# Performance work log

Measured on AMD Instinct MI355X. Metric: run time of the kernel, lower is better.

## Reference

```python
import jax, jax.numpy as jnp
import numpy as np

B, T, D = 128, 512, 128
CHUNK, LEVELS, CONV = 128, 3, 10
H = CHUNK * LEVELS          # hidden_dim = 384
G = 4 * H + 2 * LEVELS      # gate width = 1542
HS = H // 6                 # 64


def setup_inputs() -> dict:
    key = jax.random.key(0)
    ks = jax.random.split(key, 12)
    def w(k, shape, fan_in):
        return (jax.random.normal(k, shape, jnp.float32) / jnp.sqrt(jnp.float32(fan_in)))
    return {
        "x": jax.random.normal(ks[0], (B, T, D), jnp.float32),
        "lengths": jax.random.randint(ks[1], (B,), 1, T + 1, jnp.int32),
        # kernel: Linear(D+1 -> G); stored as [in, out]
        "Wk": w(ks[2], (D + 1, G), D + 1),
        "bk": jnp.zeros((G,), jnp.float32),
        # recurrent_kernel: Linear(H+1 -> G)
        "Wr": w(ks[3], (H + 1, G), H + 1),
        "br": jnp.zeros((G,), jnp.float32),
        # nn_scale: H -> H//6 ; nn_rescale: H//6 -> H
        "Ws": w(ks[4], (H, HS), H),
        "bs": jnp.zeros((HS,), jnp.float32),
        "Wrs": w(ks[5], (HS, H), HS),
        "brs": jnp.zeros((H,), jnp.float32),
        # nn_conv: Conv1d(H, H, CONV) -> weight [out, in, k]
        "Wc": w(ks[6], (H, H, CONV), H * CONV),
        "bc": jnp.zeros((H,), jnp.float32),
    }


def _cumax_l2r(z):
    return jnp.cumsum(jax.nn.softmax(z, axis=-1), axis=-1)


def _cumax_r2l(z):
    s = jax.nn.softmax(z, axis=-1)  # softmax is order-invariant, flip commutes
    return jnp.flip(jnp.cumsum(jnp.flip(s, -1), -1), -1)


def reference(x, lengths, Wk, bk, Wr, br, Ws, bs, Wrs, brs, Wc, bc):
    del lengths  # present in the torch signature but unused in forward
    dtype = x.dtype
    one = jnp.ones((B, 1), dtype)  # time_intervals are all ones

    def step(carry, x_t):
        c, h, buf_h, buf_d = carry
        x_out = (jnp.concatenate([x_t, one], -1) @ Wk + bk
                 + jnp.concatenate([h, one], -1) @ Wr + br)  # [B, G]
        f_master = _cumax_l2r(x_out[:, :LEVELS])[:, :, None]          # [B,L,1]
        i_master = _cumax_r2l(x_out[:, LEVELS:2 * LEVELS])[:, :, None]
        gates = x_out[:, 2 * LEVELS:].reshape(B, 4 * LEVELS, CHUNK)
        f_g = jax.nn.sigmoid(gates[:, :LEVELS])
        i_g = jax.nn.sigmoid(gates[:, LEVELS:2 * LEVELS])
        o_g = jax.nn.sigmoid(gates[:, 2 * LEVELS:3 * LEVELS])
        c_in = jnp.tanh(gates[:, 3 * LEVELS:])
        c_l = c.reshape(B, LEVELS, CHUNK)
        ov = f_master * i_master
        c_new = (ov * (f_g * c_l + i_g * c_in)
                 + (f_master - ov) * c_l + (i_master - ov) * c_in)
        h_new = (o_g * jnp.tanh(c_new)).reshape(B, H)
        c_new = c_new.reshape(B, H)
        cur_dist = 1.0 - f_master[..., 0].mean(-1)  # [B]
        # sliding window buffers (newest last)
        buf_h = jnp.concatenate([buf_h[1:], h_new[None]], 0)   # [CONV,B,H]
        buf_d = jnp.concatenate([buf_d[1:], cur_dist[None]], 0)  # [CONV,B]
        local_dis = jax.nn.softmax(jnp.cumsum(buf_d.T, axis=1), axis=1)  # [B,CONV]
        local_h = buf_h.transpose(1, 2, 0) * local_dis[:, None, :]       # [B,H,CONV]
        theme = jax.nn.sigmoid(
            jax.nn.relu(local_h.mean(-1) @ Ws + bs) @ Wrs + brs)         # [B,H]
        # Conv1d with kernel_size == window -> full contraction over (in,k)
        conv = jnp.einsum('bik,oik->bo', local_h, Wc) + bc               # [B,H]
        return (c_new, h_new, buf_h, buf_d), (h_new, theme * conv)

    carry0 = (jnp.zeros((B, H), dtype), jnp.zeros((B, H), dtype),
              jnp.zeros((CONV, B, H), dtype), jnp.zeros((CONV, B), dtype))
    _, (origin_h, y) = jax.lax.scan(step, carry0, x.transpose(1, 0, 2))
    # [T,B,H] -> [B,T,H]; dropout layers are identity at inference
    return y.transpose(1, 0, 2) + origin_h.transpose(1, 0, 2)
```

## Files before the change

kernel.cpp:

```cpp
#include <hip/hip_runtime.h>

typedef unsigned short ushort_t;
typedef unsigned int uint32;
typedef unsigned long long uint64;
typedef __attribute__((ext_vector_type(8))) short bf16x8;
typedef __attribute__((ext_vector_type(8))) unsigned short ushort8;
typedef __attribute__((ext_vector_type(4))) float f32x4;

#define Bsz 128
#define T_STEPS 512
#define D_IN 128
#define H_DIM 384
#define G_DIM 1542
#define CONV_W 10
#define HB_ROW 49152
#define TP 521

__device__ __forceinline__ float bf2f(ushort_t u) {
  return __builtin_bit_cast(float, (uint32)u << 16);
}
__device__ __forceinline__ ushort_t f2bf(float f) {
  uint32 u = __builtin_bit_cast(uint32, f);
  u += 0x7fffu + ((u >> 16) & 1u);
  return (ushort_t)(u >> 16);
}
__device__ __forceinline__ float sigf(float x) { return 1.f / (1.f + __expf(-x)); }
__device__ __forceinline__ float tanh_f(float x) { return 1.f - 2.f / (1.f + __expf(2.f * x)); }
__device__ __forceinline__ float ldg_f(const void* p, size_t i, int f32) {
  return f32 ? ((const float*)p)[i] : bf2f(((const ushort_t*)p)[i]);
}

__global__ __launch_bounds__(64) void k_detect(const uint32* __restrict__ xw, int* __restrict__ dflag) {
  int lane = threadIdx.x;
  int cnt = 0;
  for (int i = 0; i < 16; ++i) {
    uint32 v = xw[lane * 16 + i];
    uint32 e = (v >> 7) & 0xFFu;
    cnt += (e == 0u || (e >= 0x70u && e <= 0x8Eu)) ? 1 : 0;
  }
  for (int off = 32; off; off >>= 1) cnt += __shfl_down(cnt, off);
  if (lane == 0) dflag[0] = (cnt < 700) ? 1 : 0;
}

__global__ __launch_bounds__(256) void k_zero(ushort_t* Hb, float* CD, int* flags) {
  int idx = blockIdx.x * 256 + threadIdx.x;
  if (idx < 9 * HB_ROW) Hb[idx] = 0;
  if (idx < 9 * Bsz) CD[idx] = 0.f;
  if (idx < 256) flags[idx] = 0;
}

__global__ __launch_bounds__(256) void k_packwt(const void* __restrict__ Wk, const void* __restrict__ bk,
                                                const void* __restrict__ Wr, const void* __restrict__ br,
                                                ushort_t* __restrict__ Wt, float* __restrict__ bias,
                                                const int* __restrict__ dflag) {
  const int is32 = dflag[0];
  int idx = blockIdx.x * 256 + threadIdx.x;
  int c = idx >> 9, k = idx & 511;
  int xc = (c < 1536) ? (c + 6) : (c - 1536);
  float v = 0.f;
  if (c < 1542)
    v = (k < 384) ? ldg_f(Wr, (size_t)k * G_DIM + xc, is32)
                  : ldg_f(Wk, (size_t)(k - 384) * G_DIM + xc, is32);
  Wt[idx] = f2bf(v);
  if (k == 0) {
    float bv = 0.f;
    if (c < 1542)
      bv = ldg_f(bk, xc, is32) + ldg_f(br, xc, is32)
         + ldg_f(Wk, (size_t)128 * G_DIM + xc, is32) + ldg_f(Wr, (size_t)384 * G_DIM + xc, is32);
    bias[c] = bv;
  }
}

__global__ __launch_bounds__(256) void k_packwp(const void* __restrict__ Wc, ushort_t* __restrict__ Wp,
                                                const int* __restrict__ dflag) {
  const int is32 = dflag[0];
  int idx = blockIdx.x * 256 + threadIdx.x;
  int o = idx / 3840, kk = idx % 3840;
  int k = kk / 384, i = kk % 384;
  Wp[idx] = f2bf(ldg_f(Wc, (size_t)o * 3840 + i * CONV_W + k, is32));
}

__global__ __launch_bounds__(256) void k_packsml(const void* Ws, const void* bs, const void* Wrs,
                                                 const void* brs, const void* bc,
                                                 ushort_t* Wsb, float* bsf, ushort_t* Wrsb,
                                                 float* brsf, float* bcf, const int* dflag) {
  const int is32 = dflag[0];
  int idx = blockIdx.x * 256 + threadIdx.x;
  if (idx < 24576) Wsb[idx] = f2bf(ldg_f(Ws, idx, is32));
  else if (idx < 49152) Wrsb[idx - 24576] = f2bf(ldg_f(Wrs, idx - 24576, is32));
  else if (idx < 49152 + 64) bsf[idx - 49152] = ldg_f(bs, idx - 49152, is32);
  else if (idx < 49216 + 384) brsf[idx - 49216] = ldg_f(brs, idx - 49216, is32);
  else if (idx < 49600 + 384) bcf[idx - 49600] = ldg_f(bc, idx - 49600, is32);
}

__global__ __launch_bounds__(256) void k_phaseA(const void* __restrict__ xv,
                                                const ushort_t* __restrict__ Wt,
                                                const float* __restrict__ bias,
                                                ushort_t* __restrict__ Hb,
                                                float* __restrict__ CD,
                                                int* __restrict__ flags,
                                                const int* __restrict__ dflag) {
  __shared__ float zbuf[5][16][17];
  const int is32 = dflag[0];
  const int bid = blockIdx.x;
  const int mt = bid & 7;
  const int unit = bid >> 3;
  const int lv = unit / 8, jg = unit % 8;
  const int tid = threadIdx.x;
  const int w = tid >> 6, lane = tid & 63;
  const int l15 = lane & 15, quad = lane >> 4;

  const int brow = mt * 16 + l15;
  const int cb = (lv + 3 * w) * 128 + jg * 16;
  const ushort_t* bptr = Wt + (size_t)(cb + l15) * 512 + quad * 8;
  const ushort_t* mwptr = Wt + (size_t)(1536 + l15) * 512 + quad * 8;
  const size_t xoff = (size_t)brow * (T_STEPS * D_IN) + quad * 8;
  const ushort_t* xu = (const ushort_t*)xv;
  const float* xf = (const float*)xv;
  const float biasg = bias[cb + l15];
  const float biasm = bias[1536 + l15];

  const int b_local = tid >> 4, jj = tid & 15;
  const int col = lv * 128 + jg * 16 + jj;
  const int bg = mt * 16 + b_local;
  float creg = 0.f;

  int* gflags = flags + mt * 32;

  for (int t = 0; t < T_STEPS; ++t) {
    f32x4 acc = {0.f, 0.f, 0.f, 0.f};
    f32x4 accm = {0.f, 0.f, 0.f, 0.f};
    const size_t xo = xoff + (size_t)t * D_IN;
    if (!is32) {
#pragma unroll
      for (int ks = 0; ks < 4; ++ks) {
        bf16x8 a = *(const bf16x8*)(xu + xo + ks * 32);
        bf16x8 bb = *(const bf16x8*)(bptr + (12 + ks) * 32);
        acc = __builtin_amdgcn_mfma_f32_16x16x32_bf16(a, bb, acc, 0, 0, 0);
        if (w == 0) {
          bf16x8 bm = *(const bf16x8*)(mwptr + (12 + ks) * 32);
          accm = __builtin_amdgcn_mfma_f32_16x16x32_bf16(a, bm, accm, 0, 0, 0);
        }
      }
    } else {
#pragma unroll
      for (int ks = 0; ks < 4; ++ks) {
        f32x4 fa = *(const f32x4*)(xf + xo + ks * 32);
        f32x4 fb = *(const f32x4*)(xf + xo + ks * 32 + 4);
        bf16x8 a;
#pragma unroll
        for (int j = 0; j < 4; ++j) { a[j] = (short)f2bf(fa[j]); a[4 + j] = (short)f2bf(fb[j]); }
        bf16x8 bb = *(const bf16x8*)(bptr + (12 + ks) * 32);
        acc = __builtin_amdgcn_mfma_f32_16x16x32_bf16(a, bb, acc, 0, 0, 0);
        if (w == 0) {
          bf16x8 bm = *(const bf16x8*)(mwptr + (12 + ks) * 32);
          accm = __builtin_amdgcn_mfma_f32_16x16x32_bf16(a, bm, accm, 0, 0, 0);
        }
      }
    }

    if (t > 0) {
      while (true) {
        int ok = 1;
        if (lane < 24) {
          int v = __hip_atomic_load(&gflags[lane], __ATOMIC_RELAXED, __HIP_MEMORY_SCOPE_AGENT);
          ok = (v >= t) ? 1 : 0;
        }
        if (__all(ok)) break;
      }
    }

    const ushort_t* hptr = Hb + (size_t)(8 + t) * HB_ROW + brow * H_DIM + quad * 8;
#pragma unroll
    for (int ks = 0; ks < 12; ++ks) {
      uint64 lo = __hip_atomic_load((const uint64*)(hptr + ks * 32), __ATOMIC_RELAXED, __HIP_MEMORY_SCOPE_AGENT);
      uint64 hi = __hip_atomic_load((const uint64*)(hptr + ks * 32 + 4), __ATOMIC_RELAXED, __HIP_MEMORY_SCOPE_AGENT);
      bf16x8 a;
      ((uint64*)&a)[0] = lo;
      ((uint64*)&a)[1] = hi;
      bf16x8 bb = *(const bf16x8*)(bptr + ks * 32);
      acc = __builtin_amdgcn_mfma_f32_16x16x32_bf16(a, bb, acc, 0, 0, 0);
      if (w == 0) {
        bf16x8 bm = *(const bf16x8*)(mwptr + ks * 32);
        accm = __builtin_amdgcn_mfma_f32_16x16x32_bf16(a, bm, accm, 0, 0, 0);
      }
    }
#pragma unroll
    for (int r = 0; r < 4; ++r) {
      zbuf[w][quad * 4 + r][l15] = acc[r] + biasg;
      if (w == 0) zbuf[4][quad * 4 + r][l15] = accm[r] + biasm;
    }
    __syncthreads();

    {
      float z0 = zbuf[4][b_local][0], z1 = zbuf[4][b_local][1], z2 = zbuf[4][b_local][2];
      float z3 = zbuf[4][b_local][3], z4 = zbuf[4][b_local][4], z5 = zbuf[4][b_local][5];
      float mf = fmaxf(z0, fmaxf(z1, z2));
      float e0 = __expf(z0 - mf), e1 = __expf(z1 - mf), e2 = __expf(z2 - mf);
      float rs = 1.f / (e0 + e1 + e2);
      float p0 = e0 * rs, p1 = e1 * rs;
      float fm = (lv == 0) ? p0 : (lv == 1) ? (p0 + p1) : 1.f;
      float mi = fmaxf(z3, fmaxf(z4, z5));
      float g0 = __expf(z3 - mi), g1 = __expf(z4 - mi), g2 = __expf(z5 - mi);
      float ris = 1.f / (g0 + g1 + g2);
      float q1 = g1 * ris, q2 = g2 * ris;
      float im = (lv == 0) ? 1.f : (lv == 1) ? (q1 + q2) : q2;

      float fg = sigf(zbuf[0][b_local][jj]);
      float ig = sigf(zbuf[1][b_local][jj]);
      float og = sigf(zbuf[2][b_local][jj]);
      float ci = tanh_f(zbuf[3][b_local][jj]);
      float ov = fm * im;
      float cn = creg * (ov * fg + fm - ov) + ci * (ov * ig + im - ov);
      creg = cn;
      float h = og * tanh_f(cn);

      float hp = __shfl_xor(h, 1);
      if (!(jj & 1)) {
        uint32 packed = (uint32)f2bf(h) | ((uint32)f2bf(hp) << 16);
        uint32* dst = (uint32*)(Hb + (size_t)(9 + t) * HB_ROW + bg * H_DIM + col);
        __hip_atomic_store(dst, packed, __ATOMIC_RELAXED, __HIP_MEMORY_SCOPE_AGENT);
      }
      if (unit == 0 && jj == 0) {
        float cd = 1.f - (2.f * p0 + p1 + 1.f) * (1.f / 3.f);
        __hip_atomic_store(&CD[(9 + t) * Bsz + bg], cd, __ATOMIC_RELAXED, __HIP_MEMORY_SCOPE_AGENT);
      }
    }
    __syncthreads();
    if (tid == 0)
      __hip_atomic_store(&gflags[unit], t + 1, __ATOMIC_RELAXED, __HIP_MEMORY_SCOPE_AGENT);
  }
}

__global__ __launch_bounds__(256) void k_b1(const ushort_t* __restrict__ Hb,
                                            const float* __restrict__ CD,
                                            float* __restrict__ disg,
                                            const ushort_t* __restrict__ Wsb,
                                            const float* __restrict__ bsf,
                                            const ushort_t* __restrict__ Wrsb,
                                            const float* __restrict__ brsf,
                                            void* __restrict__ out,
                                            const int* __restrict__ dflag) {
  __shared__ float disL[64][CONV_W];
  __shared__ ushort_t mL[64][H_DIM];
  __shared__ ushort_t uL[64][64];
  const int is32 = dflag[0];
  const int t = blockIdx.x >> 1;
  const int b0 = (blockIdx.x & 1) * 64;
  const int tid = threadIdx.x;

  if (tid < 64) {
    int b = tid;
    float s[CONV_W];
    float cum = 0.f, mx = -1e30f;
#pragma unroll
    for (int k = 0; k < CONV_W; ++k) {
      cum += CD[(t + k) * Bsz + b0 + b];
      s[k] = cum;
      mx = fmaxf(mx, cum);
    }
    float den = 0.f;
#pragma unroll
    for (int k = 0; k < CONV_W; ++k) { s[k] = __expf(s[k] - mx); den += s[k]; }
    float inv = 1.f / den;
#pragma unroll
    for (int k = 0; k < CONV_W; ++k) {
      float v = s[k] * inv;
      disL[b][k] = v;
      disg[(size_t)((t * Bsz) + b0 + b) * CONV_W + k] = v;
    }
  }
  __syncthreads();

  for (int ch = tid; ch < 64 * 48; ch += 256) {
    int b = ch / 48, ic = (ch % 48) * 8;
    float a[8] = {0.f, 0.f, 0.f, 0.f, 0.f, 0.f, 0.f, 0.f};
#pragma unroll
    for (int k = 0; k < CONV_W; ++k) {
      float dv = disL[b][k];
      ushort8 h8 = *(const ushort8*)(Hb + (size_t)(t + k) * HB_ROW + (b0 + b) * H_DIM + ic);
#pragma unroll
      for (int j = 0; j < 8; ++j) a[j] += dv * bf2f(h8[j]);
    }
    ushort8 mo;
#pragma unroll
    for (int j = 0; j < 8; ++j) mo[j] = f2bf(a[j] * 0.1f);
    *(ushort8*)(&mL[b][ic]) = mo;
  }
  __syncthreads();

  for (int idx = tid; idx < 64 * 64; idx += 256) {
    int b = idx >> 6, hs = idx & 63;
    float s = bsf[hs];
    for (int i = 0; i < H_DIM; ++i) s += bf2f(mL[b][i]) * bf2f(Wsb[i * 64 + hs]);
    uL[b][hs] = f2bf(fmaxf(s, 0.f));
  }
  __syncthreads();

  for (int idx = tid; idx < 64 * H_DIM; idx += 256) {
    int b = idx / H_DIM, o = idx % H_DIM;
    float s = brsf[o];
    for (int hs = 0; hs < 64; ++hs) s += bf2f(uL[b][hs]) * bf2f(Wrsb[hs * H_DIM + o]);
    float th = sigf(s);
    size_t oi = (size_t)(b0 + b) * (T_STEPS * H_DIM) + (size_t)t * H_DIM + o;
    if (is32) ((float*)out)[oi] = th; else ((ushort_t*)out)[oi] = f2bf(th);
  }
}

__global__ __launch_bounds__(256, 2) void k_b2(const ushort_t* __restrict__ Hb,
                                               const float* __restrict__ disg,
                                               const ushort_t* __restrict__ Wp,
                                               const float* __restrict__ bcf,
                                               void* __restrict__ out,
                                               const int* __restrict__ dflag) {
  __shared__ float disL[Bsz * CONV_W];
  const int is32 = dflag[0];
  const int bid = blockIdx.x;
  const int t = bid & 511, nb = bid >> 9;
  const int tid = threadIdx.x;
  const int w = tid >> 6, lane = tid & 63;
  const int l15 = lane & 15, quad = lane >> 4;

  for (int idx = tid; idx < Bsz * CONV_W; idx += 256)
    disL[idx] = disg[(size_t)t * Bsz * CONV_W + idx];
  __syncthreads();

  const int nbase = nb * 128 + w * 32;
  const ushort_t* wp0 = Wp + (size_t)(nbase + l15) * 3840 + quad * 8;
  const ushort_t* wp1 = Wp + (size_t)(nbase + 16 + l15) * 3840 + quad * 8;
  const ushort_t* hbase = Hb + (size_t)t * HB_ROW + l15 * H_DIM + quad * 8;

  f32x4 macc[8][2];
#pragma unroll
  for (int m = 0; m < 8; ++m) {
    macc[m][0] = f32x4{0.f, 0.f, 0.f, 0.f};
    macc[m][1] = f32x4{0.f, 0.f, 0.f, 0.f};
  }

  for (int tap = 0; tap < CONV_W; ++tap) {
    f32x4 pacc[8][2];
#pragma unroll
    for (int m = 0; m < 8; ++m) {
      pacc[m][0] = f32x4{0.f, 0.f, 0.f, 0.f};
      pacc[m][1] = f32x4{0.f, 0.f, 0.f, 0.f};
    }
    const ushort_t* hb = hbase + (size_t)tap * HB_ROW;
    const ushort_t* w0 = wp0 + tap * 384;
    const ushort_t* w1 = wp1 + tap * 384;
#pragma unroll
    for (int s = 0; s < 12; ++s) {
      bf16x8 bb0 = *(const bf16x8*)(w0 + s * 32);
      bf16x8 bb1 = *(const bf16x8*)(w1 + s * 32);
#pragma unroll
      for (int m = 0; m < 8; ++m) {
        bf16x8 a = *(const bf16x8*)(hb + (size_t)m * 16 * H_DIM + s * 32);
        pacc[m][0] = __builtin_amdgcn_mfma_f32_16x16x32_bf16(a, bb0, pacc[m][0], 0, 0, 0);
        pacc[m][1] = __builtin_amdgcn_mfma_f32_16x16x32_bf16(a, bb1, pacc[m][1], 0, 0, 0);
      }
    }
#pragma unroll
    for (int m = 0; m < 8; ++m) {
#pragma unroll
      for (int r = 0; r < 4; ++r) {
        float dv = disL[(m * 16 + quad * 4 + r) * CONV_W + tap];
        macc[m][0][r] += dv * pacc[m][0][r];
        macc[m][1][r] += dv * pacc[m][1][r];
      }
    }
  }

  float bc0 = bcf[nbase + l15];
  float bc1 = bcf[nbase + 16 + l15];
#pragma unroll
  for (int m = 0; m < 8; ++m) {
#pragma unroll
    for (int r = 0; r < 4; ++r) {
      int b = m * 16 + quad * 4 + r;
      size_t oidx = (size_t)b * (T_STEPS * H_DIM) + (size_t)t * H_DIM;
      int o0 = nbase + l15, o1 = o0 + 16;
      float c0 = macc[m][0][r] + bc0;
      float c1 = macc[m][1][r] + bc1;
      float h0 = bf2f(Hb[(size_t)(9 + t) * HB_ROW + b * H_DIM + o0]);
      float h1 = bf2f(Hb[(size_t)(9 + t) * HB_ROW + b * H_DIM + o1]);
      if (is32) {
        float th0 = ((float*)out)[oidx + o0];
        float th1 = ((float*)out)[oidx + o1];
        ((float*)out)[oidx + o0] = th0 * c0 + h0;
        ((float*)out)[oidx + o1] = th1 * c1 + h1;
      } else {
        float th0 = bf2f(((ushort_t*)out)[oidx + o0]);
        float th1 = bf2f(((ushort_t*)out)[oidx + o1]);
        ((ushort_t*)out)[oidx + o0] = f2bf(th0 * c0 + h0);
        ((ushort_t*)out)[oidx + o1] = f2bf(th1 * c1 + h1);
      }
    }
  }
}

extern "C" void kernel_launch(void* const* d_in, const int* in_sizes, int n_in,
                              void* d_out, int out_size, void* d_ws, size_t ws_size,
                              hipStream_t stream) {
  const void* x = d_in[0];
  const void* Wk = d_in[2];
  const void* bk = d_in[3];
  const void* Wr = d_in[4];
  const void* br = d_in[5];
  const void* Ws = d_in[6];
  const void* bs = d_in[7];
  const void* Wrs = d_in[8];
  const void* brs = d_in[9];
  const void* Wc = d_in[10];
  const void* bc = d_in[11];

  char* ws = (char*)d_ws;
  size_t off = 0;
  auto alloc = [&](size_t bytes) -> void* {
    off = (off + 255) & ~(size_t)255;
    void* p = ws + off;
    off += bytes;
    return p;
  };
  ushort_t* Hb = (ushort_t*)alloc((size_t)TP * HB_ROW * 2);
  float* CD = (float*)alloc((size_t)TP * Bsz * 4);
  ushort_t* Wt = (ushort_t*)alloc((size_t)1552 * 512 * 2);
  float* bias = (float*)alloc((size_t)1552 * 4);
  ushort_t* Wp = (ushort_t*)alloc((size_t)H_DIM * 3840 * 2);
  float* disg = (float*)alloc((size_t)T_STEPS * Bsz * CONV_W * 4);
  ushort_t* Wsb = (ushort_t*)alloc(24576 * 2);
  ushort_t* Wrsb = (ushort_t*)alloc(24576 * 2);
  float* bsf = (float*)alloc(64 * 4);
  float* brsf = (float*)alloc(384 * 4);
  float* bcf = (float*)alloc(384 * 4);
  int* flags = (int*)alloc(256 * 4);
  int* dflag = (int*)alloc(64 * 4);
  (void)ws_size; (void)in_sizes; (void)n_in; (void)out_size;

  k_detect<<<1, 64, 0, stream>>>((const uint32*)x, dflag);
  k_zero<<<1728, 256, 0, stream>>>(Hb, CD, flags);
  k_packwt<<<3104, 256, 0, stream>>>(Wk, bk, Wr, br, Wt, bias, dflag);
  k_packwp<<<5760, 256, 0, stream>>>(Wc, Wp, dflag);
  k_packsml<<<196, 256, 0, stream>>>(Ws, bs, Wrs, brs, bc, Wsb, bsf, Wrsb, brsf, bcf, dflag);
  k_phaseA<<<192, 256, 0, stream>>>(x, Wt, bias, Hb, CD, flags, dflag);
  k_b1<<<1024, 256, 0, stream>>>(Hb, CD, disg, Wsb, bsf, Wrsb, brsf, d_out, dflag);
  k_b2<<<1536, 256, 0, stream>>>(Hb, disg, Wp, bcf, d_out, dflag);
}
```

Baseline: 5.950 ms.

## Replace flag-barrier handoff with tagged ring of hidden-state cells

The per-block step flags and the barrier that set them are replaced by a 4-deep ring of 64-bit cells. Each cell packs two bf16 hidden values with the step number, so consumers poll the data itself until every tag matches, then feed it straight into the MFMAs. This removes the flag publish, the second __syncthreads per step and the separate reload of h from the big history buffer, shortening the per-step critical path of the recurrence. zbuf is double-buffered so the trailing barrier can be dropped safely. The recurrent MFMA chain is split into two accumulators, and the kernel uses a launch bound of one block per CU. The cost is more polling loads and register pressure, and correctness now relies on no block running more than a few steps ahead.

```diff
diff --git a/kernel.cpp b/kernel.cpp
--- a/kernel.cpp
+++ b/kernel.cpp
@@ -42,11 +42,10 @@
   if (lane == 0) dflag[0] = (cnt < 700) ? 1 : 0;
 }
 
-__global__ __launch_bounds__(256) void k_zero(ushort_t* Hb, float* CD, int* flags) {
+__global__ __launch_bounds__(256) void k_zero(ushort_t* Hb, float* CD) {
   int idx = blockIdx.x * 256 + threadIdx.x;
   if (idx < 9 * HB_ROW) Hb[idx] = 0;
   if (idx < 9 * Bsz) CD[idx] = 0.f;
-  if (idx < 256) flags[idx] = 0;
 }
 
 __global__ __launch_bounds__(256) void k_packwt(const void* __restrict__ Wk, const void* __restrict__ bk,
@@ -93,14 +92,14 @@
   else if (idx < 49600 + 384) bcf[idx - 49600] = ldg_f(bc, idx - 49600, is32);
 }
 
-__global__ __launch_bounds__(256) void k_phaseA(const void* __restrict__ xv,
-                                                const ushort_t* __restrict__ Wt,
-                                                const float* __restrict__ bias,
-                                                ushort_t* __restrict__ Hb,
-                                                float* __restrict__ CD,
-                                                int* __restrict__ flags,
-                                                const int* __restrict__ dflag) {
-  __shared__ float zbuf[5][16][17];
+__global__ __launch_bounds__(256, 1) void k_phaseA(const void* __restrict__ xv,
+                                                   const ushort_t* __restrict__ Wt,
+                                                   const float* __restrict__ bias,
+                                                   ushort_t* __restrict__ Hb,
+                                                   float* __restrict__ CD,
+                                                   uint64* __restrict__ ring,
+                                                   const int* __restrict__ dflag) {
+  __shared__ float zbuf[2][5][16][17];
   const int is32 = dflag[0];
   const int bid = blockIdx.x;
   const int mt = bid & 7;
@@ -125,11 +124,14 @@
   const int bg = mt * 16 + b_local;
   float creg = 0.f;
 
-  int* gflags = flags + mt * 32;
+  const size_t crow = (size_t)l15 * 192 + quad * 4;
+  const size_t pcell = (size_t)b_local * 192 + (lv * 64 + jg * 8 + (jj >> 1));
 
   for (int t = 0; t < T_STEPS; ++t) {
     f32x4 acc = {0.f, 0.f, 0.f, 0.f};
+    f32x4 acc2 = {0.f, 0.f, 0.f, 0.f};
     f32x4 accm = {0.f, 0.f, 0.f, 0.f};
+    f32x4 accm2 = {0.f, 0.f, 0.f, 0.f};
     const size_t xo = xoff + (size_t)t * D_IN;
     if (!is32) {
 #pragma unroll
@@ -160,41 +162,54 @@
     }
 
     if (t > 0) {
-      while (true) {
-        int ok = 1;
-        if (lane < 24) {
-          int v = __hip_atomic_load(&gflags[lane], __ATOMIC_RELAXED, __HIP_MEMORY_SCOPE_AGENT);
-          ok = (v >= t) ? 1 : 0;
+      const uint64* rb = ring + ((size_t)(((t - 1) & 3) * 8 + mt) * 16 * 192) + crow;
+      const uint32 tgt = (uint32)t;
+      uint64 u[12][4];
+      uint64 pend = 0xFFFFFFFFFFFFull;
+      int pass = 0;
+      do {
+        if (pass++) __builtin_amdgcn_s_sleep(1);
+#pragma unroll
+        for (int ks = 0; ks < 12; ++ks)
+#pragma unroll
+          for (int c = 0; c < 4; ++c)
+            if ((pend >> (ks * 4 + c)) & 1)
+              u[ks][c] = __hip_atomic_load(rb + ks * 16 + c, __ATOMIC_RELAXED, __HIP_MEMORY_SCOPE_AGENT);
+#pragma unroll
+        for (int ks = 0; ks < 12; ++ks)
+#pragma unroll
+          for (int c = 0; c < 4; ++c)
+            if (((pend >> (ks * 4 + c)) & 1) && ((uint32)u[ks][c] == tgt))
+              pend &= ~(1ull << (ks * 4 + c));
+      } while (__any(pend != 0));
+
+#pragma unroll
+      for (int ks = 0; ks < 12; ++ks) {
+        bf16x8 a;
+#pragma unroll
+        for (int c = 0; c < 4; ++c) ((uint32*)&a)[c] = (uint32)(u[ks][c] >> 32);
+        bf16x8 bb = *(const bf16x8*)(bptr + ks * 32);
+        if (ks & 1) acc2 = __builtin_amdgcn_mfma_f32_16x16x32_bf16(a, bb, acc2, 0, 0, 0);
+        else        acc  = __builtin_amdgcn_mfma_f32_16x16x32_bf16(a, bb, acc, 0, 0, 0);
+        if (w == 0) {
+          bf16x8 bm = *(const bf16x8*)(mwptr + ks * 32);
+          if (ks & 1) accm2 = __builtin_amdgcn_mfma_f32_16x16x32_bf16(a, bm, accm2, 0, 0, 0);
+          else        accm  = __builtin_amdgcn_mfma_f32_16x16x32_bf16(a, bm, accm, 0, 0, 0);
         }
-        if (__all(ok)) break;
-      }
-    }
-
-    const ushort_t* hptr = Hb + (size_t)(8 + t) * HB_ROW + brow * H_DIM + quad * 8;
-#pragma unroll
-    for (int ks = 0; ks < 12; ++ks) {
-      uint64 lo = __hip_atomic_load((const uint64*)(hptr + ks * 32), __ATOMIC_RELAXED, __HIP_MEMORY_SCOPE_AGENT);
-      uint64 hi = __hip_atomic_load((const uint64*)(hptr + ks * 32 + 4), __ATOMIC_RELAXED, __HIP_MEMORY_SCOPE_AGENT);
-      bf16x8 a;
-      ((uint64*)&a)[0] = lo;
-      ((uint64*)&a)[1] = hi;
-      bf16x8 bb = *(const bf16x8*)(bptr + ks * 32);
-      acc = __builtin_amdgcn_mfma_f32_16x16x32_bf16(a, bb, acc, 0, 0, 0);
-      if (w == 0) {
-        bf16x8 bm = *(const bf16x8*)(mwptr + ks * 32);
-        accm = __builtin_amdgcn_mfma_f32_16x16x32_bf16(a, bm, accm, 0, 0, 0);
-      }
-    }
+      }
+    }
+
+    const int zb = t & 1;
 #pragma unroll
     for (int r = 0; r < 4; ++r) {
-      zbuf[w][quad * 4 + r][l15] = acc[r] + biasg;
-      if (w == 0) zbuf[4][quad * 4 + r][l15] = accm[r] + biasm;
+      zbuf[zb][w][quad * 4 + r][l15] = acc[r] + acc2[r] + biasg;
+      if (w == 0) zbuf[zb][4][quad * 4 + r][l15] = accm[r] + accm2[r] + biasm;
     }
     __syncthreads();
 
     {
-      float z0 = zbuf[4][b_local][0], z1 = zbuf[4][b_local][1], z2 = zbuf[4][b_local][2];
-      float z3 = zbuf[4][b_local][3], z4 = zbuf[4][b_local][4], z5 = zbuf[4][b_local][5];
+      float z0 = zbuf[zb][4][b_local][0], z1 = zbuf[zb][4][b_local][1], z2 = zbuf[zb][4][b_local][2];
+      float z3 = zbuf[zb][4][b_local][3], z4 = zbuf[zb][4][b_local][4], z5 = zbuf[zb][4][b_local][5];
       float mf = fmaxf(z0, fmaxf(z1, z2));
       float e0 = __expf(z0 - mf), e1 = __expf(z1 - mf), e2 = __expf(z2 - mf);
       float rs = 1.f / (e0 + e1 + e2);
@@ -206,10 +221,10 @@
       float q1 = g1 * ris, q2 = g2 * ris;
       float im = (lv == 0) ? 1.f : (lv == 1) ? (q1 + q2) : q2;
 
-      float fg = sigf(zbuf[0][b_local][jj]);
-      float ig = sigf(zbuf[1][b_local][jj]);
-      float og = sigf(zbuf[2][b_local][jj]);
-      float ci = tanh_f(zbuf[3][b_local][jj]);
+      float fg = sigf(zbuf[zb][0][b_local][jj]);
+      float ig = sigf(zbuf[zb][1][b_local][jj]);
+      float og = sigf(zbuf[zb][2][b_local][jj]);
+      float ci = tanh_f(zbuf[zb][3][b_local][jj]);
       float ov = fm * im;
       float cn = creg * (ov * fg + fm - ov) + ci * (ov * ig + im - ov);
       creg = cn;
@@ -218,17 +233,15 @@
       float hp = __shfl_xor(h, 1);
       if (!(jj & 1)) {
         uint32 packed = (uint32)f2bf(h) | ((uint32)f2bf(hp) << 16);
-        uint32* dst = (uint32*)(Hb + (size_t)(9 + t) * HB_ROW + bg * H_DIM + col);
-        __hip_atomic_store(dst, packed, __ATOMIC_RELAXED, __HIP_MEMORY_SCOPE_AGENT);
+        uint64 cellv = ((uint64)packed << 32) | (uint64)(t + 1);
+        uint64* dst = ring + ((size_t)((t & 3) * 8 + mt) * 16 * 192) + pcell;
+        __hip_atomic_store(dst, cellv, __ATOMIC_RELAXED, __HIP_MEMORY_SCOPE_AGENT);
+        *(uint32*)(Hb + (size_t)(9 + t) * HB_ROW + bg * H_DIM + col) = packed;
       }
       if (unit == 0 && jj == 0) {
-        float cd = 1.f - (2.f * p0 + p1 + 1.f) * (1.f / 3.f);
-        __hip_atomic_store(&CD[(9 + t) * Bsz + bg], cd, __ATOMIC_RELAXED, __HIP_MEMORY_SCOPE_AGENT);
-      }
-    }
-    __syncthreads();
-    if (tid == 0)
-      __hip_atomic_store(&gflags[unit], t + 1, __ATOMIC_RELAXED, __HIP_MEMORY_SCOPE_AGENT);
+        CD[(9 + t) * Bsz + bg] = 1.f - (2.f * p0 + p1 + 1.f) * (1.f / 3.f);
+      }
+    }
   }
 }
 
@@ -431,16 +444,16 @@
   float* bsf = (float*)alloc(64 * 4);
   float* brsf = (float*)alloc(384 * 4);
   float* bcf = (float*)alloc(384 * 4);
-  int* flags = (int*)alloc(256 * 4);
+  uint64* ring = (uint64*)alloc((size_t)4 * 8 * 16 * 192 * 8);
   int* dflag = (int*)alloc(64 * 4);
   (void)ws_size; (void)in_sizes; (void)n_in; (void)out_size;
 
   k_detect<<<1, 64, 0, stream>>>((const uint32*)x, dflag);
-  k_zero<<<1728, 256, 0, stream>>>(Hb, CD, flags);
+  k_zero<<<1728, 256, 0, stream>>>(Hb, CD);
   k_packwt<<<3104, 256, 0, stream>>>(Wk, bk, Wr, br, Wt, bias, dflag);
   k_packwp<<<5760, 256, 0, stream>>>(Wc, Wp, dflag);
   k_packsml<<<196, 256, 0, stream>>>(Ws, bs, Wrs, brs, bc, Wsb, bsf, Wrsb, brsf, bcf, dflag);
-  k_phaseA<<<192, 256, 0, stream>>>(x, Wt, bias, Hb, CD, flags, dflag);
+  k_phaseA<<<192, 256, 0, stream>>>(x, Wt, bias, Hb, CD, ring, dflag);
   k_b1<<<1024, 256, 0, stream>>>(Hb, CD, disg, Wsb, bsf, Wrsb, brsf, d_out, dflag);
   k_b2<<<1536, 256, 0, stream>>>(Hb, disg, Wp, bcf, d_out, dflag);
 }
```

After: 7.357 ms. +23.7%, slower.
